# Performance work log

Hardware: AMD Instinct MI355X
Metric: run time of the kernel (lower is better)

Reference implementation:

```python
import jax, jax.numpy as jnp
import numpy as np

REMOVE_FACTOR = 10000.0

def setup_inputs() -> dict:
    key = jax.random.key(0)
    k1, k2, k3, k4, k5, k6 = jax.random.split(key, 6)
    B, En, De, D_en, D_de, U = 32, 512, 64, 128, 128, 128
    return {
        "en_seq": jax.random.normal(k1, (B, En, D_en), dtype=jnp.float32),
        "de_seq": jax.random.normal(k2, (B, De, D_de), dtype=jnp.float32),
        "mask": jax.random.randint(k3, (B, En), 0, 2, dtype=jnp.int32),
        "w_en": jax.random.normal(k4, (D_en, U), dtype=jnp.float32) * (1.0 / np.sqrt(D_en)),
        "w_de": jax.random.normal(k5, (D_de, U), dtype=jnp.float32) * (1.0 / np.sqrt(D_de)),
        "nu": jax.random.normal(k6, (U, 1), dtype=jnp.float32) * (1.0 / np.sqrt(U)),
    }

def reference(en_seq, de_seq, mask, w_en, w_de, nu):
    B, En, _ = en_seq.shape
    De = de_seq.shape[1]
    m_en = mask.astype(en_seq.dtype)                      # (B, En)
    en = en_seq * m_en[:, :, None]                        # masked encoder seq
    att_en = jnp.einsum('bed,du->beu', en, w_en)          # (B, En, U)
    att_de = jnp.einsum('bdf,fu->bdu', de_seq, w_de)      # (B, De, U)
    # broadcast-add replaces the original explicit repeats: (B, De, En, U)
    co = jnp.tanh(att_en[:, None, :, :] + att_de[:, :, None, :])
    mu = jnp.einsum('bdeu,u->bde', co, nu[:, 0])          # (B, De, En)
    # Faithful reproduction of the original's flatten-layout mask bias:
    # repeat_elements(mask, De, axis=1) -> flat layout (en, de), then added
    # to mu whose flat layout is (de, en).
    bias = (jnp.repeat(m_en, De, axis=1).reshape(B, De, En) - 1.0) * REMOVE_FACTOR
    alphas = jax.nn.softmax(mu + bias, axis=-1)           # (B, De, En)
    sum_en = jnp.einsum('bde,bef->bdf', alphas, en)       # (B, De, D_en)
    return jnp.concatenate([de_seq, sum_en], axis=-1)     # (B, De, D_de + D_en)
```

## Files before the change

### kernel.cpp

```cpp
#include <hip/hip_runtime.h>


#define TWO_LOG2E 2.8853900817779268f
#define LOG2E     1.4426950408889634f

__device__ __forceinline__ float fexp2(float x){
#if __has_builtin(__builtin_amdgcn_exp2f)
  return __builtin_amdgcn_exp2f(x);
#else
  float r; asm("v_exp_f32 %0, %1" : "=v"(r) : "v"(x)); return r;
#endif
}
__device__ __forceinline__ float frcp(float x){
#if __has_builtin(__builtin_amdgcn_rcpf)
  return __builtin_amdgcn_rcpf(x);
#else
  float r; asm("v_rcp_f32 %0, %1" : "=v"(r) : "v"(x)); return r;
#endif
}

__global__ __launch_bounds__(256) void k_gemms(
    const float* __restrict__ en_seq, const float* __restrict__ de_seq,
    const float* __restrict__ w_en, const float* __restrict__ w_de,
    const int* __restrict__ mask,
    float* __restrict__ att_en, float* __restrict__ att_de_sc)
{
  __shared__ __align__(16) float Ws[128*128];
  __shared__ __align__(16) float As[32*128];
  const int bi = blockIdx.x, tid = threadIdx.x;
  const float* A; const float* W; float* O; int row0; bool masked;
  if (bi < 512) { A = en_seq; W = w_en; O = att_en;    row0 = bi*32;        masked = true;  }
  else          { A = de_seq; W = w_de; O = att_de_sc; row0 = (bi-512)*32;  masked = false; }

  const float4* W4 = (const float4*)W;
  float4* Ws4 = (float4*)Ws;
#pragma unroll
  for (int i = 0; i < 16; ++i) Ws4[tid + 256*i] = W4[tid + 256*i];
  const float4* A4 = (const float4*)(A + row0*128);
  float4* As4 = (float4*)As;
#pragma unroll
  for (int i = 0; i < 4; ++i) As4[tid + 256*i] = A4[tid + 256*i];
  __syncthreads();

  const int c0 = (tid & 31) * 4;
  const int r0 = (tid >> 5) * 4;
  float acc[4][4] = {};
  for (int k = 0; k < 128; k += 4) {
    float4 av[4], wv[4];
#pragma unroll
    for (int r = 0; r < 4; ++r) av[r] = *(const float4*)&As[(r0+r)*128 + k];
#pragma unroll
    for (int kk = 0; kk < 4; ++kk) wv[kk] = *(const float4*)&Ws[(k+kk)*128 + c0];
#pragma unroll
    for (int r = 0; r < 4; ++r) {
      const float* ar = (const float*)&av[r];
#pragma unroll
      for (int kk = 0; kk < 4; ++kk) {
        acc[r][0] = fmaf(ar[kk], wv[kk].x, acc[r][0]);
        acc[r][1] = fmaf(ar[kk], wv[kk].y, acc[r][1]);
        acc[r][2] = fmaf(ar[kk], wv[kk].z, acc[r][2]);
        acc[r][3] = fmaf(ar[kk], wv[kk].w, acc[r][3]);
      }
    }
  }
#pragma unroll
  for (int r = 0; r < 4; ++r) {
    const int row = row0 + r0 + r;
    const float m = masked ? (float)mask[row] : TWO_LOG2E;
    float4 o = { acc[r][0]*m, acc[r][1]*m, acc[r][2]*m, acc[r][3]*m };
    *(float4*)&O[row*128 + c0] = o;
  }
}

#define PAD 132
#define TILE_F4 2048

__global__ __launch_bounds__(512) void k_att(
    const float* __restrict__ att_en, const float* __restrict__ att_de_sc,
    const float* __restrict__ nu, const int* __restrict__ mask,
    const float* __restrict__ en_seq, const float* __restrict__ de_seq,
    float* __restrict__ out)
{
  __shared__ __align__(16) float smem[22656];
  float* const buf0  = smem;
  float* const buf1  = smem + 8448;
  float* const adC_s = smem + 16896;
  float* const nu2_s = smem + 17920;
  float* const m_s   = smem + 18048;
  float* const alph  = smem + 18560;
  float* const part  = smem;

  const int tid = threadIdx.x;
  const int l = tid & 63, w = tid >> 6;
  const int b = blockIdx.x >> 3, dg = blockIdx.x & 7;
  const int d = dg*8 + w;

  if (tid < 256)
    ((float4*)adC_s)[tid] = ((const float4*)(att_de_sc + (b*64 + dg*8)*128))[tid];
  if (tid >= 256 && tid < 384)
    nu2_s[tid-256] = -2.0f * nu[tid-256];
  m_s[tid] = (float)mask[b*512 + tid];

  float4 rg[4];
  const float4* AE4 = (const float4*)(att_en + (size_t)b * (512*128));
#define SLOAD(t) { _Pragma("unroll") for (int i_=0;i_<4;++i_) rg[i_] = AE4[(t)*TILE_F4 + tid + 512*i_]; }
#define SWRITE(bp) { _Pragma("unroll") for (int i_=0;i_<4;++i_){ const int f4i_ = tid + 512*i_; \
                     *(float4*)&(bp)[(f4i_>>5)*PAD + (f4i_&31)*4] = rg[i_]; } }
  SLOAD(0);
  SWRITE(buf0);
  __syncthreads();

  float snu2 = 0.f;
#pragma unroll
  for (int i = 0; i < 32; ++i) { float4 v = ((const float4*)nu2_s)[i]; snu2 += (v.x+v.y)+(v.z+v.w); }
  const float S_nu = -0.5f * snu2;

  for (int t = 0; t < 8; ++t) {
    if (t < 7) SLOAD(t+1);
    const float4* row4 = (const float4*)(((t & 1) ? buf1 : buf0) + l*PAD);
    const float4* ad4  = (const float4*)(adC_s + w*128);
    const float4* nv4  = (const float4*)nu2_s;
    float a0=0.f, a1=0.f, a2=0.f, a3=0.f;
#pragma unroll 4
    for (int uc = 0; uc < 32; ++uc) {
      float4 ae = row4[uc], ad = ad4[uc], nv = nv4[uc];
      float e0 = fexp2(fmaf(ae.x, TWO_LOG2E, ad.x));
      float e1 = fexp2(fmaf(ae.y, TWO_LOG2E, ad.y));
      float e2 = fexp2(fmaf(ae.z, TWO_LOG2E, ad.z));
      float e3 = fexp2(fmaf(ae.w, TWO_LOG2E, ad.w));
      a0 = fmaf(frcp(e0 + 1.f), nv.x, a0);
      a1 = fmaf(frcp(e1 + 1.f), nv.y, a1);
      a2 = fmaf(frcp(e2 + 1.f), nv.z, a2);
      a3 = fmaf(frcp(e3 + 1.f), nv.w, a3);
    }
    alph[w*512 + t*64 + l] = S_nu + ((a0+a1)+(a2+a3));
    if (t < 7) {
      __syncthreads();
      SWRITE(((t & 1) ? buf0 : buf1));
      __syncthreads();
    }
  }

  float v[8]; float mx = -3.0e38f;
#pragma unroll
  for (int t = 0; t < 8; ++t) {
    v[t] = alph[w*512 + t*64 + l] + (m_s[d*8 + t] - 1.f) * 10000.f;
    mx = fmaxf(mx, v[t]);
  }
#pragma unroll
  for (int off = 32; off > 0; off >>= 1) mx = fmaxf(mx, __shfl_xor(mx, off, 64));
  float s = 0.f, p[8];
#pragma unroll
  for (int t = 0; t < 8; ++t) { p[t] = fexp2((v[t]-mx)*LOG2E); s += p[t]; }
#pragma unroll
  for (int off = 32; off > 0; off >>= 1) s += __shfl_xor(s, off, 64);
  const float inv = frcp(s);
#pragma unroll
  for (int t = 0; t < 8; ++t)
    alph[w*512 + t*64 + l] = p[t]*inv*m_s[t*64 + l];
  __syncthreads();

  float acc2[8][2] = {};
  const float* enB = en_seq + (size_t)b * (512*128);
#pragma unroll 4
  for (int ei = 0; ei < 64; ++ei) {
    const int e = w*64 + ei;
    const float2 ev = *(const float2*)&enB[e*128 + l*2];
#pragma unroll
    for (int dd = 0; dd < 8; ++dd) {
      const float a = alph[dd*512 + e];
      acc2[dd][0] = fmaf(a, ev.x, acc2[dd][0]);
      acc2[dd][1] = fmaf(a, ev.y, acc2[dd][1]);
    }
  }
#pragma unroll
  for (int dd = 0; dd < 8; ++dd) {
    float2 t2 = { acc2[dd][0], acc2[dd][1] };
    *(float2*)&part[(w*8 + dd)*128 + l*2] = t2;
  }
  __syncthreads();

  const int brow = b*64 + dg*8;
#pragma unroll
  for (int ii = 0; ii < 2; ++ii) {
    const int idx = tid + ii*512;
    const int dd = idx >> 7, f = idx & 127;
    float s2 = 0.f;
#pragma unroll
    for (int ww = 0; ww < 8; ++ww) s2 += part[(ww*8 + dd)*128 + f];
    const int drow = brow + dd;
    out[drow*256 + f]       = de_seq[drow*128 + f];
    out[drow*256 + 128 + f] = s2;
  }
}

extern "C" void kernel_launch(void* const* d_in, const int* in_sizes, int n_in,
                              void* d_out, int out_size, void* d_ws, size_t ws_size,
                              hipStream_t stream) {
  const float* en_seq = (const float*)d_in[0];
  const float* de_seq = (const float*)d_in[1];
  const int*   mask   = (const int*)  d_in[2];
  const float* w_en   = (const float*)d_in[3];
  const float* w_de   = (const float*)d_in[4];
  const float* nu     = (const float*)d_in[5];
  float* out = (float*)d_out;

  float* att_en    = (float*)d_ws;
  float* att_de_sc = att_en + 32*512*128;

  k_gemms<<<576, 256, 0, stream>>>(en_seq, de_seq, w_en, w_de, mask, att_en, att_de_sc);
  k_att<<<256, 512, 0, stream>>>(att_en, att_de_sc, nu, mask, en_seq, de_seq, out);
}
```

Baseline: 153.2 us.

## Restructure attention kernel tiling, swizzle LDS, and split GEMM weight staging

The GEMM kernel now stages the weight matrix in two 64-row halves to halve its LDS footprint, and remaps block indices so batch varies fastest. The attention kernel drops its double-buffered padded tile for a single XOR-swizzled tile. It remaps lanes so each wave covers 8 decoder rows by 8 encoder rows, reads nu directly from global memory, and pads alpha with stride 513. The weighted-sum stage uses 8-wide float4 register tiles with shuffle reductions and float4 output writes. Lower LDS use should raise occupancy, but the single buffer adds a barrier per tile and removes the overlap of loads with compute.

Result: faster. 132.4 us (-13.6%).

```diff
diff --git a/kernel.cpp b/kernel.cpp
--- a/kernel.cpp
+++ b/kernel.cpp
@@ -25,41 +25,48 @@
     const int* __restrict__ mask,
     float* __restrict__ att_en, float* __restrict__ att_de_sc)
 {
-  __shared__ __align__(16) float Ws[128*128];
+  __shared__ __align__(16) float Ws[64*128];
   __shared__ __align__(16) float As[32*128];
   const int bi = blockIdx.x, tid = threadIdx.x;
   const float* A; const float* W; float* O; int row0; bool masked;
-  if (bi < 512) { A = en_seq; W = w_en; O = att_en;    row0 = bi*32;        masked = true;  }
-  else          { A = de_seq; W = w_de; O = att_de_sc; row0 = (bi-512)*32;  masked = false; }
-
-  const float4* W4 = (const float4*)W;
-  float4* Ws4 = (float4*)Ws;
-#pragma unroll
-  for (int i = 0; i < 16; ++i) Ws4[tid + 256*i] = W4[tid + 256*i];
+  if (bi < 512) { int b = bi & 31, j = bi >> 5;
+                  A = en_seq; W = w_en; O = att_en;    row0 = b*512 + j*32; masked = true; }
+  else          { int q = bi - 512; int b = q & 31, jj = q >> 5;
+                  A = de_seq; W = w_de; O = att_de_sc; row0 = b*64 + jj*32; masked = false; }
+
   const float4* A4 = (const float4*)(A + row0*128);
   float4* As4 = (float4*)As;
 #pragma unroll
   for (int i = 0; i < 4; ++i) As4[tid + 256*i] = A4[tid + 256*i];
-  __syncthreads();
 
   const int c0 = (tid & 31) * 4;
   const int r0 = (tid >> 5) * 4;
   float acc[4][4] = {};
-  for (int k = 0; k < 128; k += 4) {
-    float4 av[4], wv[4];
-#pragma unroll
-    for (int r = 0; r < 4; ++r) av[r] = *(const float4*)&As[(r0+r)*128 + k];
-#pragma unroll
-    for (int kk = 0; kk < 4; ++kk) wv[kk] = *(const float4*)&Ws[(k+kk)*128 + c0];
-#pragma unroll
-    for (int r = 0; r < 4; ++r) {
-      const float* ar = (const float*)&av[r];
-#pragma unroll
-      for (int kk = 0; kk < 4; ++kk) {
-        acc[r][0] = fmaf(ar[kk], wv[kk].x, acc[r][0]);
-        acc[r][1] = fmaf(ar[kk], wv[kk].y, acc[r][1]);
-        acc[r][2] = fmaf(ar[kk], wv[kk].z, acc[r][2]);
-        acc[r][3] = fmaf(ar[kk], wv[kk].w, acc[r][3]);
+
+  for (int ph = 0; ph < 2; ++ph) {
+    if (ph) __syncthreads();
+    const float4* W4 = (const float4*)(W + ph*64*128);
+    float4* Ws4 = (float4*)Ws;
+#pragma unroll
+    for (int i = 0; i < 8; ++i) Ws4[tid + 256*i] = W4[tid + 256*i];
+    __syncthreads();
+    for (int k = 0; k < 64; k += 4) {
+      const int kg = ph*64 + k;
+      float4 av[4], wv[4];
+#pragma unroll
+      for (int r = 0; r < 4; ++r) av[r] = *(const float4*)&As[(r0+r)*128 + kg];
+#pragma unroll
+      for (int kk = 0; kk < 4; ++kk) wv[kk] = *(const float4*)&Ws[(k+kk)*128 + c0];
+#pragma unroll
+      for (int r = 0; r < 4; ++r) {
+        const float* ar = (const float*)&av[r];
+#pragma unroll
+        for (int kk = 0; kk < 4; ++kk) {
+          acc[r][0] = fmaf(ar[kk], wv[kk].x, acc[r][0]);
+          acc[r][1] = fmaf(ar[kk], wv[kk].y, acc[r][1]);
+          acc[r][2] = fmaf(ar[kk], wv[kk].z, acc[r][2]);
+          acc[r][3] = fmaf(ar[kk], wv[kk].w, acc[r][3]);
+        }
       }
     }
   }
@@ -71,9 +78,6 @@
     *(float4*)&O[row*128 + c0] = o;
   }
 }
-
-#define PAD 132
-#define TILE_F4 2048
 
 __global__ __launch_bounds__(512) void k_att(
     const float* __restrict__ att_en, const float* __restrict__ att_de_sc,
@@ -81,49 +85,50 @@
     const float* __restrict__ en_seq, const float* __restrict__ de_seq,
     float* __restrict__ out)
 {
-  __shared__ __align__(16) float smem[22656];
-  float* const buf0  = smem;
-  float* const buf1  = smem + 8448;
-  float* const adC_s = smem + 16896;
-  float* const nu2_s = smem + 17920;
-  float* const m_s   = smem + 18048;
-  float* const alph  = smem + 18560;
-  float* const part  = smem;
+  __shared__ __align__(16) float smem[13864];
+  float* const tile = smem;
+  float* const alph = smem + 8192;
+  float* const m_s  = smem + 12296;
+  float* const adC  = smem + 12808;
+  float* const part = smem;
 
   const int tid = threadIdx.x;
   const int l = tid & 63, w = tid >> 6;
-  const int b = blockIdx.x >> 3, dg = blockIdx.x & 7;
-  const int d = dg*8 + w;
-
-  if (tid < 256)
-    ((float4*)adC_s)[tid] = ((const float4*)(att_de_sc + (b*64 + dg*8)*128))[tid];
-  if (tid >= 256 && tid < 384)
-    nu2_s[tid-256] = -2.0f * nu[tid-256];
+  const int b = blockIdx.x & 31, dg = blockIdx.x >> 5;
+
+  if (tid < 256) {
+    const int row = tid >> 5, q = tid & 31;
+    *(float4*)&adC[row*132 + q*4] =
+        *(const float4*)&att_de_sc[(b*64 + dg*8 + row)*128 + q*4];
+  }
   m_s[tid] = (float)mask[b*512 + tid];
+
+  float snu = nu[l] + nu[l + 64];
+#pragma unroll
+  for (int off = 32; off > 0; off >>= 1) snu += __shfl_xor(snu, off, 64);
+  const float S_nu = snu;
 
   float4 rg[4];
   const float4* AE4 = (const float4*)(att_en + (size_t)b * (512*128));
-#define SLOAD(t) { _Pragma("unroll") for (int i_=0;i_<4;++i_) rg[i_] = AE4[(t)*TILE_F4 + tid + 512*i_]; }
-#define SWRITE(bp) { _Pragma("unroll") for (int i_=0;i_<4;++i_){ const int f4i_ = tid + 512*i_; \
-                     *(float4*)&(bp)[(f4i_>>5)*PAD + (f4i_&31)*4] = rg[i_]; } }
+#define SLOAD(t) { _Pragma("unroll") for (int i_=0;i_<4;++i_) rg[i_] = AE4[(t)*2048 + tid + 512*i_]; }
+#define SWRITE() { _Pragma("unroll") for (int i_=0;i_<4;++i_){ const int f4i_ = tid + 512*i_; \
+                   const int row_ = f4i_>>5, q_ = f4i_&31; \
+                   *(float4*)&tile[row_*128 + ((q_ ^ (row_&7))<<2)] = rg[i_]; } }
   SLOAD(0);
-  SWRITE(buf0);
+  SWRITE();
   __syncthreads();
 
-  float snu2 = 0.f;
-#pragma unroll
-  for (int i = 0; i < 32; ++i) { float4 v = ((const float4*)nu2_s)[i]; snu2 += (v.x+v.y)+(v.z+v.w); }
-  const float S_nu = -0.5f * snu2;
-
+  const int dP = l & 7, er = l >> 3;
+  const int r  = w*8 + er;
+  const float* adrow = adC + dP*132;
   for (int t = 0; t < 8; ++t) {
     if (t < 7) SLOAD(t+1);
-    const float4* row4 = (const float4*)(((t & 1) ? buf1 : buf0) + l*PAD);
-    const float4* ad4  = (const float4*)(adC_s + w*128);
-    const float4* nv4  = (const float4*)nu2_s;
     float a0=0.f, a1=0.f, a2=0.f, a3=0.f;
 #pragma unroll 4
     for (int uc = 0; uc < 32; ++uc) {
-      float4 ae = row4[uc], ad = ad4[uc], nv = nv4[uc];
+      float4 ae = *(const float4*)&tile[r*128 + ((uc ^ (r&7))<<2)];
+      float4 ad = *(const float4*)&adrow[uc<<2];
+      float4 nv = *(const float4*)&nu[uc<<2];
       float e0 = fexp2(fmaf(ae.x, TWO_LOG2E, ad.x));
       float e1 = fexp2(fmaf(ae.y, TWO_LOG2E, ad.y));
       float e2 = fexp2(fmaf(ae.z, TWO_LOG2E, ad.z));
@@ -133,18 +138,15 @@
       a2 = fmaf(frcp(e2 + 1.f), nv.z, a2);
       a3 = fmaf(frcp(e3 + 1.f), nv.w, a3);
     }
-    alph[w*512 + t*64 + l] = S_nu + ((a0+a1)+(a2+a3));
-    if (t < 7) {
-      __syncthreads();
-      SWRITE(((t & 1) ? buf0 : buf1));
-      __syncthreads();
-    }
+    alph[dP*513 + t*64 + w*8 + er] = (a0+a1)+(a2+a3);
+    __syncthreads();
+    if (t < 7) { SWRITE(); __syncthreads(); }
   }
 
   float v[8]; float mx = -3.0e38f;
 #pragma unroll
   for (int t = 0; t < 8; ++t) {
-    v[t] = alph[w*512 + t*64 + l] + (m_s[d*8 + t] - 1.f) * 10000.f;
+    v[t] = S_nu - 2.f*alph[w*513 + t*64 + l] + (m_s[dg*64 + w*8 + t] - 1.f) * 10000.f;
     mx = fmaxf(mx, v[t]);
   }
 #pragma unroll
@@ -157,40 +159,58 @@
   const float inv = frcp(s);
 #pragma unroll
   for (int t = 0; t < 8; ++t)
-    alph[w*512 + t*64 + l] = p[t]*inv*m_s[t*64 + l];
+    alph[w*513 + t*64 + l] = p[t]*inv*m_s[t*64 + l];
   __syncthreads();
 
-  float acc2[8][2] = {};
+  const int f0 = (l & 15) * 8, es = l >> 4;
+  float acc2[8][8] = {};
   const float* enB = en_seq + (size_t)b * (512*128);
-#pragma unroll 4
-  for (int ei = 0; ei < 64; ++ei) {
-    const int e = w*64 + ei;
-    const float2 ev = *(const float2*)&enB[e*128 + l*2];
+  for (int it = 0; it < 16; ++it) {
+    const int e = w*64 + it*4 + es;
+    float4 ev0 = *(const float4*)&enB[e*128 + f0];
+    float4 ev1 = *(const float4*)&enB[e*128 + f0 + 4];
 #pragma unroll
     for (int dd = 0; dd < 8; ++dd) {
-      const float a = alph[dd*512 + e];
-      acc2[dd][0] = fmaf(a, ev.x, acc2[dd][0]);
-      acc2[dd][1] = fmaf(a, ev.y, acc2[dd][1]);
-    }
-  }
-#pragma unroll
-  for (int dd = 0; dd < 8; ++dd) {
-    float2 t2 = { acc2[dd][0], acc2[dd][1] };
-    *(float2*)&part[(w*8 + dd)*128 + l*2] = t2;
+      const float a = alph[dd*513 + e];
+      acc2[dd][0] = fmaf(a, ev0.x, acc2[dd][0]);
+      acc2[dd][1] = fmaf(a, ev0.y, acc2[dd][1]);
+      acc2[dd][2] = fmaf(a, ev0.z, acc2[dd][2]);
+      acc2[dd][3] = fmaf(a, ev0.w, acc2[dd][3]);
+      acc2[dd][4] = fmaf(a, ev1.x, acc2[dd][4]);
+      acc2[dd][5] = fmaf(a, ev1.y, acc2[dd][5]);
+      acc2[dd][6] = fmaf(a, ev1.z, acc2[dd][6]);
+      acc2[dd][7] = fmaf(a, ev1.w, acc2[dd][7]);
+    }
+  }
+#pragma unroll
+  for (int dd = 0; dd < 8; ++dd)
+#pragma unroll
+    for (int j = 0; j < 8; ++j) {
+      acc2[dd][j] += __shfl_xor(acc2[dd][j], 16, 64);
+      acc2[dd][j] += __shfl_xor(acc2[dd][j], 32, 64);
+    }
+  if (l < 16) {
+#pragma unroll
+    for (int dd = 0; dd < 8; ++dd) {
+      float4 t0 = { acc2[dd][0], acc2[dd][1], acc2[dd][2], acc2[dd][3] };
+      float4 t1 = { acc2[dd][4], acc2[dd][5], acc2[dd][6], acc2[dd][7] };
+      *(float4*)&part[(w*8 + dd)*128 + f0]     = t0;
+      *(float4*)&part[(w*8 + dd)*128 + f0 + 4] = t1;
+    }
   }
   __syncthreads();
 
-  const int brow = b*64 + dg*8;
-#pragma unroll
-  for (int ii = 0; ii < 2; ++ii) {
-    const int idx = tid + ii*512;
-    const int dd = idx >> 7, f = idx & 127;
-    float s2 = 0.f;
-#pragma unroll
-    for (int ww = 0; ww < 8; ++ww) s2 += part[(ww*8 + dd)*128 + f];
-    const int drow = brow + dd;
-    out[drow*256 + f]       = de_seq[drow*128 + f];
-    out[drow*256 + 128 + f] = s2;
+  if (tid < 256) {
+    const int dd = tid >> 5, fq = (tid & 31) * 4;
+    float4 s2 = {0.f, 0.f, 0.f, 0.f};
+#pragma unroll
+    for (int ww = 0; ww < 8; ++ww) {
+      float4 pv = *(const float4*)&part[(ww*8 + dd)*128 + fq];
+      s2.x += pv.x; s2.y += pv.y; s2.z += pv.z; s2.w += pv.w;
+    }
+    const int drow = b*64 + dg*8 + dd;
+    *(float4*)&out[drow*256 + fq]       = *(const float4*)&de_seq[drow*128 + fq];
+    *(float4*)&out[drow*256 + 128 + fq] = s2;
   }
 }
 
```
